# Optimization experiments

Measured on AMD Instinct MI355X. Metric: run time of the kernel, lower is better.

## Reference

```python
import jax, jax.numpy as jnp
import numpy as np

D = 512          # hidden_dim
NH = 8           # num_heads
DH = D // NH     # head dim
N = 100000       # num_nodes
C = 64           # context size
E = 1600000      # num_edges (unused in math, required by signature)
LN_EPS = 1e-5


def layer_norm(x, g, b):
    mu = jnp.mean(x, axis=-1, keepdims=True)
    var = jnp.var(x, axis=-1, keepdims=True)
    return (x - mu) * jax.lax.rsqrt(var + LN_EPS) * g + b


def mha(q, kv, W_in, b_in, W_out, b_out):
    # torch nn.MultiheadAttention (batch of 1 folded out). q:[Lq,D], kv:[Lk,D]
    Wq, Wk, Wv = jnp.split(W_in, 3, axis=0)
    bq, bk, bv = jnp.split(b_in, 3)
    qh = (q @ Wq.T + bq).reshape(-1, NH, DH)
    kh = (kv @ Wk.T + bk).reshape(-1, NH, DH)
    vh = (kv @ Wv.T + bv).reshape(-1, NH, DH)
    scores = jnp.einsum('qhd,khd->hqk', qh, kh) * (DH ** -0.5)
    w = jax.nn.softmax(scores, axis=-1)
    out = jnp.einsum('hqk,khd->qhd', w, vh).reshape(-1, D)
    return out @ W_out.T + b_out


def setup_inputs() -> dict:
    key = jax.random.key(0)
    ks = jax.random.split(key, 12)
    s = 0.02
    return {
        'H': jax.random.normal(ks[0], (N, D), jnp.float32),
        'path_token': jax.random.normal(ks[1], (D,), jnp.float32),
        'W_in1': jax.random.normal(ks[2], (3 * D, D), jnp.float32) * s,
        'b_in1': jnp.zeros((3 * D,), jnp.float32),
        'W_out1': jax.random.normal(ks[3], (D, D), jnp.float32) * s,
        'b_out1': jnp.zeros((D,), jnp.float32),
        'W_in2': jax.random.normal(ks[4], (3 * D, D), jnp.float32) * s,
        'b_in2': jnp.zeros((3 * D,), jnp.float32),
        'W_out2': jax.random.normal(ks[5], (D, D), jnp.float32) * s,
        'b_out2': jnp.zeros((D,), jnp.float32),
        'ln1_g': jnp.ones((D,), jnp.float32),
        'ln1_b': jnp.zeros((D,), jnp.float32),
        'ln2_g': jnp.ones((D,), jnp.float32),
        'ln2_b': jnp.zeros((D,), jnp.float32),
        'edge_index': jax.random.randint(ks[6], (2, E), 0, N, jnp.int64)
            if jax.config.jax_enable_x64 else jax.random.randint(ks[6], (2, E), 0, N, jnp.int32),
        'context_ids': jax.random.randint(ks[7], (C,), 0, N, jnp.int32),
    }


def reference(H, path_token, W_in1, b_in1, W_out1, b_out1,
              W_in2, b_in2, W_out2, b_out2,
              ln1_g, ln1_b, ln2_g, ln2_b,
              edge_index, context_ids):
    # gather context node reprs [C, D]
    ctx = H[context_ids]
    # path attention: 1 query (path token) over C context keys/values
    upd = mha(path_token[None, :], ctx, W_in1, b_in1, W_out1, b_out1)[0]
    upd = layer_norm(upd + path_token, ln1_g, ln1_b)  # [D]
    # graph attention: every node queries N identical copies of `upd`.
    # All logits per query are equal -> softmax exactly uniform -> per-head
    # output == v_head(upd). So attn_out = out_proj(v_proj(upd)), identical
    # for every node (exact, not approximate).
    _, _, Wv2 = jnp.split(W_in2, 3, axis=0)
    bv2 = b_in2[2 * D:]
    v = upd @ Wv2.T + bv2                       # [D]
    attn2 = v @ W_out2.T + b_out2               # [D], broadcast over nodes
    H_cond = layer_norm(attn2[None, :] + H, ln2_g, ln2_b)  # [N, D]
    return H_cond
```

## Files before the change

kernel.cpp:

```cpp
#include <hip/hip_runtime.h>

#define D 512
#define NH 8
#define DH 64
#define CCTX 64
#define LN_EPS 1e-5f

#define WS_QH    0
#define WS_T     512
#define WS_M     1024
#define WS_CTX   5120
#define WS_CBAR  37888
#define WS_O     41984
#define WS_OUT1  42496
#define WS_V     43008
#define WS_ATTN2 43520

__device__ __forceinline__ float waveReduceSum(float v) {
#pragma unroll
    for (int off = 32; off > 0; off >>= 1) v += __shfl_xor(v, off);
    return v;
}

__global__ __launch_bounds__(256) void k_qh_gather(
    const float* __restrict__ Win1, const float* __restrict__ bin1,
    const float* __restrict__ path, const float* __restrict__ Hm,
    const int* __restrict__ ids, float* __restrict__ ws)
{
    if (blockIdx.x < 128) {
        int wid  = blockIdx.x * 4 + (threadIdx.x >> 6);
        int lane = threadIdx.x & 63;
        const float* Wr = Win1 + (size_t)wid * D;
        float4 w0 = *(const float4*)(Wr + lane * 4);
        float4 w1 = *(const float4*)(Wr + 256 + lane * 4);
        float4 x0 = *(const float4*)(path + lane * 4);
        float4 x1 = *(const float4*)(path + 256 + lane * 4);
        float s = w0.x*x0.x + w0.y*x0.y + w0.z*x0.z + w0.w*x0.w
                + w1.x*x1.x + w1.y*x1.y + w1.z*x1.z + w1.w*x1.w;
        s = waveReduceSum(s);
        if (lane == 0) ws[WS_QH + wid] = s + bin1[wid];
    } else {
        int j = blockIdx.x - 128;
        if (threadIdx.x < 128) {
            int id = ids[j];
            float4 v = *(const float4*)(Hm + (size_t)id * D + threadIdx.x * 4);
            *(float4*)(ws + WS_CTX + j * D + threadIdx.x * 4) = v;
        }
    }
}

__global__ __launch_bounds__(256) void k_m(
    const float* __restrict__ Win1, const float* __restrict__ bin1,
    float* __restrict__ ws)
{
    int idx = blockIdx.x * 256 + threadIdx.x;
    int h = idx >> 9;
    int c = idx & (D - 1);
    const float* Wk = Win1 + D * D;
    const float* q  = ws + WS_QH + h * DH;
    float acc = 0.f;
#pragma unroll 8
    for (int d = 0; d < DH; ++d) acc += Wk[(h * DH + d) * D + c] * q[d];
    ws[WS_M + idx] = acc;
    if (c == 0) {
        const float* bk = bin1 + D + h * DH;
        float tt = 0.f;
        for (int d = 0; d < DH; ++d) tt += bk[d] * q[d];
        ws[WS_T + h] = tt;
    }
}

__global__ __launch_bounds__(512) void k_attn(float* __restrict__ ws)
{
    __shared__ float s_lds[NH][CCTX];
    __shared__ float w_lds[NH][CCTX];
    int tid = threadIdx.x;

    {
        int j = tid >> 3, h = tid & 7;
        const float* cr = ws + WS_CTX + j * D;
        const float* mr = ws + WS_M + h * D;
        float s = 0.f;
#pragma unroll 4
        for (int c4 = 0; c4 < 128; ++c4) {
            float4 a = *(const float4*)(cr + c4 * 4);
            float4 b = *(const float4*)(mr + c4 * 4);
            s += a.x*b.x + a.y*b.y + a.z*b.z + a.w*b.w;
        }
        s_lds[h][j] = (s + ws[WS_T + h]) * 0.125f;
    }
    __syncthreads();

    {
        int h = tid >> 6, j = tid & 63;
        float sc = s_lds[h][j];
        float mx = sc;
#pragma unroll
        for (int off = 32; off > 0; off >>= 1) mx = fmaxf(mx, __shfl_xor(mx, off));
        float e = __expf(sc - mx);
        float sum = waveReduceSum(e);
        w_lds[h][j] = e / sum;
    }
    __syncthreads();

    {
        int c = tid;
        float acc[NH];
#pragma unroll
        for (int h = 0; h < NH; ++h) acc[h] = 0.f;
        for (int j = 0; j < CCTX; ++j) {
            float x = ws[WS_CTX + j * D + c];
#pragma unroll
            for (int h = 0; h < NH; ++h) acc[h] += w_lds[h][j] * x;
        }
#pragma unroll
        for (int h = 0; h < NH; ++h) ws[WS_CBAR + h * D + c] = acc[h];
    }
}

__global__ __launch_bounds__(256) void k_matvec(
    const float* __restrict__ W, const float* __restrict__ x,
    const float* __restrict__ b, float* __restrict__ y, int headStride)
{
    int wid  = blockIdx.x * 4 + (threadIdx.x >> 6);
    int lane = threadIdx.x & 63;
    const float* xr = x + (wid >> 6) * headStride;
    const float* Wr = W + (size_t)wid * D;
    float4 w0 = *(const float4*)(Wr + lane * 4);
    float4 w1 = *(const float4*)(Wr + 256 + lane * 4);
    float4 x0 = *(const float4*)(xr + lane * 4);
    float4 x1 = *(const float4*)(xr + 256 + lane * 4);
    float s = w0.x*x0.x + w0.y*x0.y + w0.z*x0.z + w0.w*x0.w
            + w1.x*x1.x + w1.y*x1.y + w1.z*x1.z + w1.w*x1.w;
    s = waveReduceSum(s);
    if (lane == 0) y[wid] = s + b[wid];
}

__global__ __launch_bounds__(256) void k_matvec_ln(
    const float* __restrict__ W, const float* __restrict__ pre,
    const float* __restrict__ addv, const float* __restrict__ g,
    const float* __restrict__ bln, const float* __restrict__ b,
    float* __restrict__ y)
{
    __shared__ __align__(16) float xs[D];
    __shared__ float red[8];
    int tid = threadIdx.x;
    float a0 = pre[tid * 2]     + addv[tid * 2];
    float a1 = pre[tid * 2 + 1] + addv[tid * 2 + 1];
    float s  = a0 + a1;
    float s2 = a0 * a0 + a1 * a1;
    s  = waveReduceSum(s);
    s2 = waveReduceSum(s2);
    int wib = tid >> 6, lane = tid & 63;
    if (lane == 0) { red[wib] = s; red[4 + wib] = s2; }
    __syncthreads();
    float st  = red[0] + red[1] + red[2] + red[3];
    float s2t = red[4] + red[5] + red[6] + red[7];
    float mu   = st * (1.f / D);
    float var  = s2t * (1.f / D) - mu * mu;
    float rinv = rsqrtf(var + LN_EPS);
    xs[tid * 2]     = (a0 - mu) * rinv * g[tid * 2]     + bln[tid * 2];
    xs[tid * 2 + 1] = (a1 - mu) * rinv * g[tid * 2 + 1] + bln[tid * 2 + 1];
    __syncthreads();
    int wid = blockIdx.x * 4 + wib;
    const float* Wr = W + (size_t)wid * D;
    float4 w0 = *(const float4*)(Wr + lane * 4);
    float4 w1 = *(const float4*)(Wr + 256 + lane * 4);
    float4 x0 = *(const float4*)(xs + lane * 4);
    float4 x1 = *(const float4*)(xs + 256 + lane * 4);
    float sd = w0.x*x0.x + w0.y*x0.y + w0.z*x0.z + w0.w*x0.w
             + w1.x*x1.x + w1.y*x1.y + w1.z*x1.z + w1.w*x1.w;
    sd = waveReduceSum(sd);
    if (lane == 0) y[wid] = sd + b[wid];
}

__global__ __launch_bounds__(256) void k_final(
    const float* __restrict__ Hm, const float* __restrict__ attn2,
    const float* __restrict__ g, const float* __restrict__ b,
    float* __restrict__ out, int N)
{
    int lane = threadIdx.x & 63;
    int wib  = threadIdx.x >> 6;
    int c0 = lane * 4, c1 = 256 + lane * 4;
    float4 a0 = *(const float4*)(attn2 + c0), a1 = *(const float4*)(attn2 + c1);
    float4 g0 = *(const float4*)(g + c0),     g1 = *(const float4*)(g + c1);
    float4 b0 = *(const float4*)(b + c0),     b1 = *(const float4*)(b + c1);
    int stride = gridDim.x * 4;
    for (int row = blockIdx.x * 4 + wib; row < N; row += stride) {
        const float* hr = Hm + (size_t)row * D;
        float4 x0 = *(const float4*)(hr + c0);
        float4 x1 = *(const float4*)(hr + c1);
        x0.x += a0.x; x0.y += a0.y; x0.z += a0.z; x0.w += a0.w;
        x1.x += a1.x; x1.y += a1.y; x1.z += a1.z; x1.w += a1.w;
        float s  = x0.x + x0.y + x0.z + x0.w + x1.x + x1.y + x1.z + x1.w;
        float s2 = x0.x*x0.x + x0.y*x0.y + x0.z*x0.z + x0.w*x0.w
                 + x1.x*x1.x + x1.y*x1.y + x1.z*x1.z + x1.w*x1.w;
#pragma unroll
        for (int off = 32; off > 0; off >>= 1) {
            s  += __shfl_xor(s, off);
            s2 += __shfl_xor(s2, off);
        }
        float mu   = s * (1.f / D);
        float var  = s2 * (1.f / D) - mu * mu;
        float rinv = rsqrtf(var + LN_EPS);
        float4 y0, y1;
        y0.x = (x0.x - mu) * rinv * g0.x + b0.x;
        y0.y = (x0.y - mu) * rinv * g0.y + b0.y;
        y0.z = (x0.z - mu) * rinv * g0.z + b0.z;
        y0.w = (x0.w - mu) * rinv * g0.w + b0.w;
        y1.x = (x1.x - mu) * rinv * g1.x + b1.x;
        y1.y = (x1.y - mu) * rinv * g1.y + b1.y;
        y1.z = (x1.z - mu) * rinv * g1.z + b1.z;
        y1.w = (x1.w - mu) * rinv * g1.w + b1.w;
        float* orow = out + (size_t)row * D;
        *(float4*)(orow + c0) = y0;
        *(float4*)(orow + c1) = y1;
    }
}

extern "C" void kernel_launch(void* const* d_in, const int* in_sizes, int n_in,
                              void* d_out, int out_size, void* d_ws, size_t ws_size,
                              hipStream_t stream)
{
    const float* Hm    = (const float*)d_in[0];
    const float* path  = (const float*)d_in[1];
    const float* Win1  = (const float*)d_in[2];
    const float* bin1  = (const float*)d_in[3];
    const float* Wout1 = (const float*)d_in[4];
    const float* bout1 = (const float*)d_in[5];
    const float* Win2  = (const float*)d_in[6];
    const float* bin2  = (const float*)d_in[7];
    const float* Wout2 = (const float*)d_in[8];
    const float* bout2 = (const float*)d_in[9];
    const float* ln1g  = (const float*)d_in[10];
    const float* ln1b  = (const float*)d_in[11];
    const float* ln2g  = (const float*)d_in[12];
    const float* ln2b  = (const float*)d_in[13];
    const int*   ids   = (const int*)d_in[15];

    float* ws  = (float*)d_ws;
    float* out = (float*)d_out;
    const int N = in_sizes[0] / D;

    k_qh_gather<<<192, 256, 0, stream>>>(Win1, bin1, path, Hm, ids, ws);
    k_m<<<16, 256, 0, stream>>>(Win1, bin1, ws);
    k_attn<<<1, 512, 0, stream>>>(ws);
    k_matvec<<<128, 256, 0, stream>>>(Win1 + 2 * D * D, ws + WS_CBAR,
                                      bin1 + 2 * D, ws + WS_O, D);
    k_matvec<<<128, 256, 0, stream>>>(Wout1, ws + WS_O, bout1, ws + WS_OUT1, 0);
    k_matvec_ln<<<128, 256, 0, stream>>>(Win2 + 2 * D * D, ws + WS_OUT1, path,
                                         ln1g, ln1b, bin2 + 2 * D, ws + WS_V);
    k_matvec<<<128, 256, 0, stream>>>(Wout2, ws + WS_V, bout2, ws + WS_ATTN2, 0);
    k_final<<<2048, 256, 0, stream>>>(Hm, ws + WS_ATTN2, ln2g, ln2b, out, N);
}
```

Baseline: 144.6 us.

## Fuse small-vector chain into one persistent kernel with grid barriers

Replaces seven small dependent launches (q projection, gather, key fold, attention, four matvecs) with one 128-block kernel that separates stages with an atomic-counter grid barrier. The q projection is recomputed per head block alongside the key fold. The final LayerNorm kernel also switches to nontemporal stores for the large output. This targets launch gaps between tiny kernels, but relies on all 128 blocks being co-resident for the spin barrier and adds an init launch.

```diff
diff --git a/kernel.cpp b/kernel.cpp
--- a/kernel.cpp
+++ b/kernel.cpp
@@ -5,16 +5,19 @@
 #define DH 64
 #define CCTX 64
 #define LN_EPS 1e-5f
-
-#define WS_QH    0
-#define WS_T     512
-#define WS_M     1024
+#define NCHAIN 128
+
+#define WS_T     0
+#define WS_M     512
 #define WS_CTX   5120
-#define WS_CBAR  37888
-#define WS_O     41984
-#define WS_OUT1  42496
-#define WS_V     43008
-#define WS_ATTN2 43520
+#define WS_CBAR  40960
+#define WS_O     45056
+#define WS_OUT1  45568
+#define WS_V     46080
+#define WS_ATTN2 46592
+#define WS_BAR   47104
+
+typedef float f4v __attribute__((ext_vector_type(4)));
 
 __device__ __forceinline__ float waveReduceSum(float v) {
 #pragma unroll
@@ -22,110 +25,33 @@
     return v;
 }
 
-__global__ __launch_bounds__(256) void k_qh_gather(
-    const float* __restrict__ Win1, const float* __restrict__ bin1,
-    const float* __restrict__ path, const float* __restrict__ Hm,
-    const int* __restrict__ ids, float* __restrict__ ws)
-{
-    if (blockIdx.x < 128) {
-        int wid  = blockIdx.x * 4 + (threadIdx.x >> 6);
-        int lane = threadIdx.x & 63;
-        const float* Wr = Win1 + (size_t)wid * D;
-        float4 w0 = *(const float4*)(Wr + lane * 4);
-        float4 w1 = *(const float4*)(Wr + 256 + lane * 4);
-        float4 x0 = *(const float4*)(path + lane * 4);
-        float4 x1 = *(const float4*)(path + 256 + lane * 4);
-        float s = w0.x*x0.x + w0.y*x0.y + w0.z*x0.z + w0.w*x0.w
-                + w1.x*x1.x + w1.y*x1.y + w1.z*x1.z + w1.w*x1.w;
-        s = waveReduceSum(s);
-        if (lane == 0) ws[WS_QH + wid] = s + bin1[wid];
-    } else {
-        int j = blockIdx.x - 128;
-        if (threadIdx.x < 128) {
-            int id = ids[j];
-            float4 v = *(const float4*)(Hm + (size_t)id * D + threadIdx.x * 4);
-            *(float4*)(ws + WS_CTX + j * D + threadIdx.x * 4) = v;
-        }
-    }
-}
-
-__global__ __launch_bounds__(256) void k_m(
-    const float* __restrict__ Win1, const float* __restrict__ bin1,
-    float* __restrict__ ws)
-{
-    int idx = blockIdx.x * 256 + threadIdx.x;
-    int h = idx >> 9;
-    int c = idx & (D - 1);
-    const float* Wk = Win1 + D * D;
-    const float* q  = ws + WS_QH + h * DH;
-    float acc = 0.f;
-#pragma unroll 8
-    for (int d = 0; d < DH; ++d) acc += Wk[(h * DH + d) * D + c] * q[d];
-    ws[WS_M + idx] = acc;
-    if (c == 0) {
-        const float* bk = bin1 + D + h * DH;
-        float tt = 0.f;
-        for (int d = 0; d < DH; ++d) tt += bk[d] * q[d];
-        ws[WS_T + h] = tt;
-    }
-}
-
-__global__ __launch_bounds__(512) void k_attn(float* __restrict__ ws)
-{
-    __shared__ float s_lds[NH][CCTX];
-    __shared__ float w_lds[NH][CCTX];
-    int tid = threadIdx.x;
-
-    {
-        int j = tid >> 3, h = tid & 7;
-        const float* cr = ws + WS_CTX + j * D;
-        const float* mr = ws + WS_M + h * D;
-        float s = 0.f;
-#pragma unroll 4
-        for (int c4 = 0; c4 < 128; ++c4) {
-            float4 a = *(const float4*)(cr + c4 * 4);
-            float4 b = *(const float4*)(mr + c4 * 4);
-            s += a.x*b.x + a.y*b.y + a.z*b.z + a.w*b.w;
-        }
-        s_lds[h][j] = (s + ws[WS_T + h]) * 0.125f;
-    }
+__device__ __forceinline__ void bar128(unsigned* bar) {
     __syncthreads();
-
-    {
-        int h = tid >> 6, j = tid & 63;
-        float sc = s_lds[h][j];
-        float mx = sc;
-#pragma unroll
-        for (int off = 32; off > 0; off >>= 1) mx = fmaxf(mx, __shfl_xor(mx, off));
-        float e = __expf(sc - mx);
-        float sum = waveReduceSum(e);
-        w_lds[h][j] = e / sum;
+    if (threadIdx.x == 0) {
+        unsigned g = __hip_atomic_load(&bar[1], __ATOMIC_RELAXED, __HIP_MEMORY_SCOPE_AGENT);
+        unsigned old = __hip_atomic_fetch_add(&bar[0], 1u, __ATOMIC_ACQ_REL, __HIP_MEMORY_SCOPE_AGENT);
+        if (old == (unsigned)(NCHAIN - 1)) {
+            __hip_atomic_store(&bar[0], 0u, __ATOMIC_RELAXED, __HIP_MEMORY_SCOPE_AGENT);
+            __hip_atomic_store(&bar[1], g + 1u, __ATOMIC_RELEASE, __HIP_MEMORY_SCOPE_AGENT);
+        } else {
+            while (__hip_atomic_load(&bar[1], __ATOMIC_ACQUIRE, __HIP_MEMORY_SCOPE_AGENT) == g) {}
+        }
     }
     __syncthreads();
-
-    {
-        int c = tid;
-        float acc[NH];
-#pragma unroll
-        for (int h = 0; h < NH; ++h) acc[h] = 0.f;
-        for (int j = 0; j < CCTX; ++j) {
-            float x = ws[WS_CTX + j * D + c];
-#pragma unroll
-            for (int h = 0; h < NH; ++h) acc[h] += w_lds[h][j] * x;
-        }
-#pragma unroll
-        for (int h = 0; h < NH; ++h) ws[WS_CBAR + h * D + c] = acc[h];
-    }
-}
-
-__global__ __launch_bounds__(256) void k_matvec(
+}
+
+__global__ __launch_bounds__(64) void k_init(unsigned* bar) {
+    if (threadIdx.x < 2) bar[threadIdx.x] = 0u;
+}
+
+__device__ __forceinline__ void matvec_rows(
     const float* __restrict__ W, const float* __restrict__ x,
     const float* __restrict__ b, float* __restrict__ y, int headStride)
 {
-    int wid  = blockIdx.x * 4 + (threadIdx.x >> 6);
-    int lane = threadIdx.x & 63;
-    const float* xr = x + (wid >> 6) * headStride;
-    const float* Wr = W + (size_t)wid * D;
+    int wib = threadIdx.x >> 6, lane = threadIdx.x & 63;
+    int r = blockIdx.x * 4 + wib;
+    const float* xr = x + (r >> 6) * headStride;
+    const float* Wr = W + (size_t)r * D;
     float4 w0 = *(const float4*)(Wr + lane * 4);
     float4 w1 = *(const float4*)(Wr + 256 + lane * 4);
     float4 x0 = *(const float4*)(xr + lane * 4);
@@ -133,45 +59,140 @@
     float s = w0.x*x0.x + w0.y*x0.y + w0.z*x0.z + w0.w*x0.w
             + w1.x*x1.x + w1.y*x1.y + w1.z*x1.z + w1.w*x1.w;
     s = waveReduceSum(s);
-    if (lane == 0) y[wid] = s + b[wid];
-}
-
-__global__ __launch_bounds__(256) void k_matvec_ln(
-    const float* __restrict__ W, const float* __restrict__ pre,
-    const float* __restrict__ addv, const float* __restrict__ g,
-    const float* __restrict__ bln, const float* __restrict__ b,
-    float* __restrict__ y)
-{
-    __shared__ __align__(16) float xs[D];
-    __shared__ float red[8];
-    int tid = threadIdx.x;
-    float a0 = pre[tid * 2]     + addv[tid * 2];
-    float a1 = pre[tid * 2 + 1] + addv[tid * 2 + 1];
-    float s  = a0 + a1;
-    float s2 = a0 * a0 + a1 * a1;
-    s  = waveReduceSum(s);
-    s2 = waveReduceSum(s2);
-    int wib = tid >> 6, lane = tid & 63;
-    if (lane == 0) { red[wib] = s; red[4 + wib] = s2; }
-    __syncthreads();
-    float st  = red[0] + red[1] + red[2] + red[3];
-    float s2t = red[4] + red[5] + red[6] + red[7];
-    float mu   = st * (1.f / D);
-    float var  = s2t * (1.f / D) - mu * mu;
-    float rinv = rsqrtf(var + LN_EPS);
-    xs[tid * 2]     = (a0 - mu) * rinv * g[tid * 2]     + bln[tid * 2];
-    xs[tid * 2 + 1] = (a1 - mu) * rinv * g[tid * 2 + 1] + bln[tid * 2 + 1];
-    __syncthreads();
-    int wid = blockIdx.x * 4 + wib;
-    const float* Wr = W + (size_t)wid * D;
-    float4 w0 = *(const float4*)(Wr + lane * 4);
-    float4 w1 = *(const float4*)(Wr + 256 + lane * 4);
-    float4 x0 = *(const float4*)(xs + lane * 4);
-    float4 x1 = *(const float4*)(xs + 256 + lane * 4);
-    float sd = w0.x*x0.x + w0.y*x0.y + w0.z*x0.z + w0.w*x0.w
-             + w1.x*x1.x + w1.y*x1.y + w1.z*x1.z + w1.w*x1.w;
-    sd = waveReduceSum(sd);
-    if (lane == 0) y[wid] = sd + b[wid];
+    if (lane == 0) y[r] = s + b[r];
+}
+
+__global__ __launch_bounds__(256) void k_chain(
+    const float* __restrict__ Hm,   const float* __restrict__ path,
+    const float* __restrict__ Win1, const float* __restrict__ bin1,
+    const float* __restrict__ Wout1,const float* __restrict__ bout1,
+    const float* __restrict__ Win2, const float* __restrict__ bin2,
+    const float* __restrict__ Wout2,const float* __restrict__ bout2,
+    const float* __restrict__ ln1g, const float* __restrict__ ln1b,
+    const int* __restrict__ ids,    float* __restrict__ ws)
+{
+    __shared__ __align__(16) float smem[1040];
+    unsigned* bar = (unsigned*)(ws + WS_BAR);
+    const int B = blockIdx.x, tid = threadIdx.x;
+    const int wib = tid >> 6, lane = tid & 63;
+
+    if (B < 64) {
+        if (tid < 128) {
+            int id = ids[B];
+            float4 v = *(const float4*)(Hm + (size_t)id * D + tid * 4);
+            *(float4*)(ws + WS_CTX + B * D + tid * 4) = v;
+        }
+    } else if (B < 80) {
+        int bm = B - 64;
+        int h = bm >> 1, half = bm & 1;
+        float* qh_lds = smem;
+        {
+            int r = tid >> 2, p = tid & 3;
+            const float* wrow = Win1 + (size_t)(h * DH + r) * D + p * 128;
+            const float* xrow = path + p * 128;
+            float s = 0.f;
+#pragma unroll 8
+            for (int k = 0; k < 32; ++k) {
+                float4 a = *(const float4*)(wrow + k * 4);
+                float4 c = *(const float4*)(xrow + k * 4);
+                s += a.x*c.x + a.y*c.y + a.z*c.z + a.w*c.w;
+            }
+            s += __shfl_xor(s, 1);
+            s += __shfl_xor(s, 2);
+            if (p == 0) qh_lds[r] = s + bin1[h * DH + r];
+        }
+        __syncthreads();
+        {
+            int c = half * 256 + tid;
+            const float* Wk = Win1 + (size_t)D * D;
+            float acc = 0.f;
+#pragma unroll 8
+            for (int d = 0; d < DH; ++d)
+                acc += Wk[(size_t)(h * DH + d) * D + c] * qh_lds[d];
+            ws[WS_M + h * D + c] = acc;
+        }
+        if (half == 0 && tid == 0) {
+            float tt = 0.f;
+            for (int d = 0; d < DH; ++d) tt += bin1[D + h * DH + d] * qh_lds[d];
+            ws[WS_T + h] = tt;
+        }
+    }
+    bar128(bar);
+
+    if (B == 0) {
+        float* s_lds = smem;
+        float* w_lds = smem + 512;
+        for (int pidx = tid; pidx < 512; pidx += 256) {
+            int j = pidx >> 3, h = pidx & 7;
+            const float* cr = ws + WS_CTX + j * D;
+            const float* mr = ws + WS_M + h * D;
+            float s = 0.f;
+#pragma unroll 4
+            for (int c4 = 0; c4 < 128; ++c4) {
+                float4 a = *(const float4*)(cr + c4 * 4);
+                float4 b = *(const float4*)(mr + c4 * 4);
+                s += a.x*b.x + a.y*b.y + a.z*b.z + a.w*b.w;
+            }
+            s_lds[h * 64 + j] = (s + ws[WS_T + h]) * 0.125f;
+        }
+        __syncthreads();
+#pragma unroll
+        for (int hh = 0; hh < 2; ++hh) {
+            int h = wib * 2 + hh;
+            float sc = s_lds[h * 64 + lane];
+            float mx = sc;
+#pragma unroll
+            for (int off = 32; off > 0; off >>= 1) mx = fmaxf(mx, __shfl_xor(mx, off));
+            float e = __expf(sc - mx);
+            float sum = waveReduceSum(e);
+            w_lds[h * 64 + lane] = e / sum;
+        }
+        __syncthreads();
+        for (int c = tid; c < 512; c += 256) {
+            float acc[NH];
+#pragma unroll
+            for (int h = 0; h < NH; ++h) acc[h] = 0.f;
+            for (int j = 0; j < CCTX; ++j) {
+                float x = ws[WS_CTX + j * D + c];
+#pragma unroll
+                for (int h = 0; h < NH; ++h) acc[h] += w_lds[h * 64 + j] * x;
+            }
+#pragma unroll
+            for (int h = 0; h < NH; ++h) ws[WS_CBAR + h * D + c] = acc[h];
+        }
+    }
+    bar128(bar);
+
+    matvec_rows(Win1 + 2 * (size_t)D * D, ws + WS_CBAR, bin1 + 2 * D, ws + WS_O, D);
+    bar128(bar);
+
+    matvec_rows(Wout1, ws + WS_O, bout1, ws + WS_OUT1, 0);
+    bar128(bar);
+
+    {
+        float* xs  = smem;
+        float* red = smem + 520;
+        float a0 = ws[WS_OUT1 + tid * 2]     + path[tid * 2];
+        float a1 = ws[WS_OUT1 + tid * 2 + 1] + path[tid * 2 + 1];
+        float s  = a0 + a1;
+        float s2 = a0 * a0 + a1 * a1;
+        s  = waveReduceSum(s);
+        s2 = waveReduceSum(s2);
+        if (lane == 0) { red[wib] = s; red[4 + wib] = s2; }
+        __syncthreads();
+        float st  = red[0] + red[1] + red[2] + red[3];
+        float s2t = red[4] + red[5] + red[6] + red[7];
+        float mu   = st * (1.f / D);
+        float var  = s2t * (1.f / D) - mu * mu;
+        float rinv = rsqrtf(var + LN_EPS);
+        xs[tid * 2]     = (a0 - mu) * rinv * ln1g[tid * 2]     + ln1b[tid * 2];
+        xs[tid * 2 + 1] = (a1 - mu) * rinv * ln1g[tid * 2 + 1] + ln1b[tid * 2 + 1];
+        __syncthreads();
+        matvec_rows(Win2 + 2 * (size_t)D * D, xs, bin2 + 2 * D, ws + WS_V, 0);
+    }
+    bar128(bar);
+
+    matvec_rows(Wout2, ws + WS_V, bout2, ws + WS_ATTN2, 0);
 }
 
 __global__ __launch_bounds__(256) void k_final(
@@ -203,7 +224,7 @@
         float mu   = s * (1.f / D);
         float var  = s2 * (1.f / D) - mu * mu;
         float rinv = rsqrtf(var + LN_EPS);
-        float4 y0, y1;
+        f4v y0, y1;
         y0.x = (x0.x - mu) * rinv * g0.x + b0.x;
         y0.y = (x0.y - mu) * rinv * g0.y + b0.y;
         y0.z = (x0.z - mu) * rinv * g0.z + b0.z;
@@ -213,8 +234,8 @@
         y1.z = (x1.z - mu) * rinv * g1.z + b1.z;
         y1.w = (x1.w - mu) * rinv * g1.w + b1.w;
         float* orow = out + (size_t)row * D;
-        *(float4*)(orow + c0) = y0;
-        *(float4*)(orow + c1) = y1;
+        __builtin_nontemporal_store(y0, (f4v*)(orow + c0));
+        __builtin_nontemporal_store(y1, (f4v*)(orow + c1));
     }
 }
 
@@ -242,14 +263,9 @@
     float* out = (float*)d_out;
     const int N = in_sizes[0] / D;
 
-    k_qh_gather<<<192, 256, 0, stream>>>(Win1, bin1, path, Hm, ids, ws);
-    k_m<<<16, 256, 0, stream>>>(Win1, bin1, ws);
-    k_attn<<<1, 512, 0, stream>>>(ws);
-    k_matvec<<<128, 256, 0, stream>>>(Win1 + 2 * D * D, ws + WS_CBAR,
-                                      bin1 + 2 * D, ws + WS_O, D);
-    k_matvec<<<128, 256, 0, stream>>>(Wout1, ws + WS_O, bout1, ws + WS_OUT1, 0);
-    k_matvec_ln<<<128, 256, 0, stream>>>(Win2 + 2 * D * D, ws + WS_OUT1, path,
-                                         ln1g, ln1b, bin2 + 2 * D, ws + WS_V);
-    k_matvec<<<128, 256, 0, stream>>>(Wout2, ws + WS_V, bout2, ws + WS_ATTN2, 0);
+    k_init<<<1, 64, 0, stream>>>((unsigned*)(ws + WS_BAR));
+    k_chain<<<NCHAIN, 256, 0, stream>>>(Hm, path, Win1, bin1, Wout1, bout1,
+                                        Win2, bin2, Wout2, bout2, ln1g, ln1b,
+                                        ids, ws);
     k_final<<<2048, 256, 0, stream>>>(Hm, ws + WS_ATTN2, ln2g, ln2b, out, N);
 }
```

New measurement: 212.2 us. +46.8%, slower.
